# Kernel tuning notes

Hardware: AMD Instinct MI355X
Metric: run time of the kernel (lower is better)

## Reference

```python
import jax, jax.numpy as jnp
import numpy as np

B, N, D, H, MLP = 8, 1024, 1024, 16, 4096
DEPTH = D // H
EPS = 1e-6
INV_SQRT_DEPTH = 1.0 / np.sqrt(DEPTH).astype(np.float32)


def _linear_params(key, fan_in, fan_out):
    w = jax.random.normal(key, (fan_in, fan_out), dtype=jnp.float32) * 0.02
    b = jnp.zeros((fan_out,), dtype=jnp.float32)
    return w, b


def setup_inputs() -> dict:
    key = jax.random.key(0)
    ks = jax.random.split(key, 20)
    inp = {}
    inp['inputs'] = jax.random.normal(ks[0], (B, N, D), dtype=jnp.float32)
    inp['z'] = jax.random.normal(ks[1], (B, D), dtype=jnp.float32)
    # norm1 conditioning MLPs
    inp['n1_hw'], inp['n1_hb'] = _linear_params(ks[2], D, D)
    inp['n1_gw'], inp['n1_gb'] = _linear_params(ks[3], D, D)
    inp['n1_bw'], inp['n1_bb'] = _linear_params(ks[4], D, D)
    # attention
    inp['wq_w'], inp['wq_b'] = _linear_params(ks[5], D, D)
    inp['wk_w'], inp['wk_b'] = _linear_params(ks[6], D, D)
    inp['wv_w'], inp['wv_b'] = _linear_params(ks[7], D, D)
    inp['qa_w'], inp['qa_b'] = _linear_params(ks[8], D, H)
    inp['out_w'], inp['out_b'] = _linear_params(ks[9], D, D)
    # norm2 conditioning MLPs
    inp['n2_hw'], inp['n2_hb'] = _linear_params(ks[10], D, D)
    inp['n2_gw'], inp['n2_gb'] = _linear_params(ks[11], D, D)
    inp['n2_bw'], inp['n2_bb'] = _linear_params(ks[12], D, D)
    # MLP
    inp['mlp_w1'], inp['mlp_b1'] = _linear_params(ks[13], D, MLP)
    inp['mlp_w2'], inp['mlp_b2'] = _linear_params(ks[14], MLP, D)
    return inp


def _sm_norm(x, z, hw, hb, gw, gb, bw, bb):
    # LayerNorm over last dim, no affine
    mean = jnp.mean(x, axis=-1, keepdims=True)
    var = jnp.mean(jnp.square(x - mean), axis=-1, keepdims=True)
    xn = (x - mean) / jnp.sqrt(var + EPS)
    h = jax.nn.relu(z @ hw + hb)                 # [B, D]
    scale = (h @ gw + gb)[:, :, None]            # [B, D, 1]
    shift = (h @ bw + bb)[:, :, None]            # [B, D, 1]
    # broadcasts since N == D (as in the torch module)
    return xn * scale + shift


def _additive_attn(x, wq_w, wq_b, wk_w, wk_b, wv_w, wv_b, qa_w, qa_b, out_w, out_b):
    q = x @ wq_w + wq_b                          # [B, N, D]
    k = x @ wk_w + wk_b
    v = x @ wv_w + wv_b
    attn = jnp.transpose(q @ qa_w + qa_b, (0, 2, 1)) * INV_SQRT_DEPTH  # [B, H, N]
    attn = jax.nn.softmax(attn, axis=-1)
    qh = q.reshape(B, N, H, DEPTH).transpose(0, 2, 1, 3)  # [B, H, N, d]
    kh = k.reshape(B, N, H, DEPTH).transpose(0, 2, 1, 3)
    vh = v.reshape(B, N, H, DEPTH).transpose(0, 2, 1, 3)
    global_q = jnp.einsum('bhn,bhnd->bhd', attn, qh)[:, :, None, :]  # [B, H, 1, d]
    r = global_q * kh * vh                       # [B, H, N, d]
    r = r.transpose(0, 2, 1, 3).reshape(B, N, D)
    return r @ out_w + out_b, attn


def reference(inputs, z,
              n1_hw, n1_hb, n1_gw, n1_gb, n1_bw, n1_bb,
              wq_w, wq_b, wk_w, wk_b, wv_w, wv_b, qa_w, qa_b, out_w, out_b,
              n2_hw, n2_hb, n2_gw, n2_gb, n2_bw, n2_bb,
              mlp_w1, mlp_b1, mlp_w2, mlp_b2):
    x_norm1 = _sm_norm(inputs, z, n1_hw, n1_hb, n1_gw, n1_gb, n1_bw, n1_bb)
    attn_out, attn_maps = _additive_attn(x_norm1, wq_w, wq_b, wk_w, wk_b,
                                         wv_w, wv_b, qa_w, qa_b, out_w, out_b)
    attn_out = inputs + attn_out                 # dropout rate 0 -> identity
    x_norm2 = _sm_norm(attn_out, z, n2_hw, n2_hb, n2_gw, n2_gb, n2_bw, n2_bb)
    h = jax.nn.gelu(x_norm2 @ mlp_w1 + mlp_b1, approximate=False)
    mlp_out = h @ mlp_w2 + mlp_b2
    output = attn_out + mlp_out
    return output, attn_maps
```

## Files before the change

### kernel.cpp

```cpp
#include <hip/hip_runtime.h>
#include <math.h>


typedef __attribute__((ext_vector_type(8))) short short8;
typedef __attribute__((ext_vector_type(4))) float f32x4;

#define DEVI __device__ __forceinline__

DEVI unsigned short f2bf(float f) {
  union { float f; unsigned int u; } c; c.f = f;
  unsigned int r = c.u + 0x7fffu + ((c.u >> 16) & 1u);
  return (unsigned short)(r >> 16);
}
DEVI float bf2f(unsigned short u) {
  union { unsigned int u; float f; } c; c.u = ((unsigned int)u) << 16;
  return c.f;
}

DEVI void async16(const void* g, void* l) {
  __builtin_amdgcn_global_load_lds((const __attribute__((address_space(1))) void*)g,
                                   (__attribute__((address_space(3))) void*)l, 16, 0, 0);
}

__global__ void transpose_bf16_k(const float* __restrict__ in,
                                 unsigned short* __restrict__ out, int R, int C) {
  __shared__ float tile[32][33];
  const int c0 = blockIdx.x * 32, r0 = blockIdx.y * 32;
  const int tx = threadIdx.x, ty = threadIdx.y;
#pragma unroll
  for (int j = 0; j < 4; j++) {
    int r = r0 + ty + j * 8, c = c0 + tx;
    if (r < R && c < C) tile[ty + j * 8][tx] = in[(size_t)r * C + c];
  }
  __syncthreads();
#pragma unroll
  for (int j = 0; j < 4; j++) {
    int c = c0 + ty + j * 8, r = r0 + tx;
    if (c < C && r < R) out[(size_t)c * R + r] = f2bf(tile[tx][ty + j * 8]);
  }
}

__global__ void pad_bias_k(const float* __restrict__ qa_b, float* __restrict__ pad) {
  int t = threadIdx.x;
  pad[t] = (t < 16) ? qa_b[t] : 0.f;
}

__global__ void bias3_k(const float* __restrict__ b0, const float* __restrict__ b1,
                        const float* __restrict__ b2, float* __restrict__ out) {
  const int t = blockIdx.x * 256 + threadIdx.x;
  out[t] = (t < 1024) ? b0[t] : (t < 2048 ? b1[t - 1024] : b2[t - 2048]);
}

__global__ void zero_k(float4* __restrict__ p) {
  p[blockIdx.x * 256 + threadIdx.x] = float4{0.f, 0.f, 0.f, 0.f};
}

template <int NMAT>
__global__ __launch_bounds__(256) void skinny_k(const float* __restrict__ X,
                                                const float* __restrict__ W0,
                                                const float* __restrict__ W1,
                                                float* __restrict__ acc0,
                                                float* __restrict__ acc1) {
  const int tid = threadIdx.x;
  const int jt = blockIdx.x, kc = blockIdx.y;
  const int jl = tid & 63, kg = tid >> 6;
  const int jcol = jt * 64 + jl;
  __shared__ float xs[8][64];
  for (int i = tid; i < 512; i += 256) {
    const int b = i >> 6, kk = i & 63;
    xs[b][kk] = X[b * 1024 + kc * 64 + kk];
  }
  __syncthreads();
  float a0[8], a1[8];
#pragma unroll
  for (int b = 0; b < 8; b++) { a0[b] = 0.f; a1[b] = 0.f; }
#pragma unroll
  for (int kk = 0; kk < 16; kk++) {
    const int k = kg * 16 + kk;
    const float w0 = W0[(size_t)(kc * 64 + k) * 1024 + jcol];
#pragma unroll
    for (int b = 0; b < 8; b++) a0[b] += xs[b][k] * w0;
    if (NMAT == 2) {
      const float w1 = W1[(size_t)(kc * 64 + k) * 1024 + jcol];
#pragma unroll
      for (int b = 0; b < 8; b++) a1[b] += xs[b][k] * w1;
    }
  }
  __shared__ float red[256][9];
#pragma unroll
  for (int b = 0; b < 8; b++) red[tid][b] = a0[b];
  __syncthreads();
  if (tid < 64) {
#pragma unroll
    for (int b = 0; b < 8; b++) {
      const float s = red[tid][b] + red[tid + 64][b] + red[tid + 128][b] + red[tid + 192][b];
      atomicAdd(&acc0[b * 1024 + jcol], s);
    }
  }
  if (NMAT == 2) {
    __syncthreads();
#pragma unroll
    for (int b = 0; b < 8; b++) red[tid][b] = a1[b];
    __syncthreads();
    if (tid < 64) {
#pragma unroll
      for (int b = 0; b < 8; b++) {
        const float s = red[tid][b] + red[tid + 64][b] + red[tid + 128][b] + red[tid + 192][b];
        atomicAdd(&acc1[b * 1024 + jcol], s);
      }
    }
  }
}

__global__ void h_epi_k(const float* __restrict__ acc, const float* __restrict__ hb,
                        float* __restrict__ h) {
  const int i = blockIdx.x * 256 + threadIdx.x;
  h[i] = fmaxf(acc[i] + hb[i & 1023], 0.f);
}

__global__ __launch_bounds__(256) void ln_mod_k(const float* __restrict__ x,
                                                const float* __restrict__ s_acc,
                                                const float* __restrict__ t_acc,
                                                const float* __restrict__ gb,
                                                const float* __restrict__ bb,
                                                unsigned short* __restrict__ out) {
  const int lane = threadIdx.x & 63, wid = threadIdx.x >> 6;
  const size_t row = (size_t)blockIdx.x * 4 + wid;
  const int n = (int)(row & 1023);
  const float4* xr = (const float4*)(x + row * 1024);
  float4 v[4];
  float s = 0.f, ss = 0.f;
#pragma unroll
  for (int j = 0; j < 4; j++) {
    v[j] = xr[j * 64 + lane];
    s += v[j].x + v[j].y + v[j].z + v[j].w;
    ss += v[j].x * v[j].x + v[j].y * v[j].y + v[j].z * v[j].z + v[j].w * v[j].w;
  }
#pragma unroll
  for (int o = 32; o > 0; o >>= 1) { s += __shfl_xor(s, o); ss += __shfl_xor(ss, o); }
  const float mean = s * (1.f / 1024.f);
  const float var = ss * (1.f / 1024.f) - mean * mean;
  const float inv = rsqrtf(var + 1e-6f);
  const float scale = s_acc[row] + gb[n];
  const float shift = t_acc[row] + bb[n];
  const float sc = scale * inv;
  const float sh = shift - mean * sc;
#pragma unroll
  for (int j = 0; j < 4; j++) {
    ushort4 o4;
    o4.x = f2bf(v[j].x * sc + sh);
    o4.y = f2bf(v[j].y * sc + sh);
    o4.z = f2bf(v[j].z * sc + sh);
    o4.w = f2bf(v[j].w * sc + sh);
    *(ushort4*)(out + row * 1024 + (size_t)(j * 64 + lane) * 4) = o4;
  }
}

template <int EPI, int BM>
__global__ __launch_bounds__(512, 2) void gemm256(const unsigned short* __restrict__ A,
                                                  const unsigned short* __restrict__ BT,
                                                  const float* __restrict__ bias,
                                                  const float* __restrict__ resid,
                                                  void* __restrict__ Cout,
                                                  int M, int N, int K) {
  constexpr bool SWAP = (EPI == 0 || EPI == 1);
  constexpr int WROWS = BM / 2;
  constexpr int MF = WROWS / 16;
  constexpr int MPH = MF / 2;
  constexpr int ALOADS_H = (WROWS * 64) / (512 * 8);
  __shared__ unsigned short lds[2 * BM * 64 + 2 * 256 * 64];
  unsigned short* As0 = lds;
  unsigned short* Bs0 = lds + 2 * BM * 64;
  const int tid = threadIdx.x;
  const int lane = tid & 63, w = tid >> 6;
  const int wm = w >> 2, wn = w & 3;
  const int lr = lane & 15;
  const int g0 = lane >> 4;
  const size_t brow = (size_t)blockIdx.y * BM;
  const size_t bcol = (size_t)blockIdx.x * 256;
  const unsigned short* Ab = A + brow * (size_t)K;
  const unsigned short* Bb = BT + bcol * (size_t)K;
  const int NT = K >> 6;

  const f32x4 zero = {0.f, 0.f, 0.f, 0.f};
  f32x4 acc[MF][4];
#pragma unroll
  for (int m = 0; m < MF; m++)
#pragma unroll
    for (int n = 0; n < 4; n++) acc[m][n] = zero;

  auto stageA = [&](int t, int h) {
    const int d = t & 1, k0 = t << 6;
#pragma unroll
    for (int i = 0; i < ALOADS_H; i++) {
      const int c = i * 512 + tid;
      const int r = h * WROWS + (c >> 3), g = c & 7;
      const int gl = g ^ (r & 7);
      async16(Ab + (size_t)r * K + (k0 + gl * 8),
              &As0[(size_t)d * BM * 64 + (size_t)h * WROWS * 64 + c * 8]);
    }
  };
  auto stageB = [&](int t, int h) {
    const int d = t & 1, k0 = t << 6;
#pragma unroll
    for (int i = 0; i < 2; i++) {
      const int c = i * 512 + tid;
      const int r = h * 128 + (c >> 3), g = c & 7;
      const int gl = g ^ (r & 7);
      async16(Bb + (size_t)r * K + (k0 + gl * 8),
              &Bs0[(size_t)d * 256 * 64 + (size_t)h * 128 * 64 + c * 8]);
    }
  };

  stageA(0, 0); stageA(0, 1); stageB(0, 0); stageB(0, 1);

  for (int t = 0; t < NT; ++t) {
    const unsigned short* as = As0 + (size_t)(t & 1) * BM * 64;
    const unsigned short* bs = Bs0 + (size_t)(t & 1) * 256 * 64;
#pragma unroll
    for (int p = 0; p < 4; ++p) {
      if (t + 1 < NT) {
        if (p == 0) stageA(t + 1, 0);
        else if (p == 1) stageA(t + 1, 1);
        else if (p == 2) stageB(t + 1, 0);
        else stageB(t + 1, 1);
      }
      if (p == 0) {
        if (t + 1 < NT) {
          if constexpr (ALOADS_H == 2) asm volatile("s_waitcnt vmcnt(2)" ::: "memory");
          else asm volatile("s_waitcnt vmcnt(1)" ::: "memory");
        } else {
          asm volatile("s_waitcnt vmcnt(0)" ::: "memory");
        }
        __builtin_amdgcn_s_barrier();
      }
      const int mf0 = (p >> 1) * MPH;
      const int nf0 = (p & 1) * 2;
      short8 bfrag[2][2], afrag[2][MPH];
#pragma unroll
      for (int kki = 0; kki < 2; kki++) {
        const int gk = kki * 4 + g0;
#pragma unroll
        for (int nf = 0; nf < 2; nf++) {
          const int r = wn * 64 + (nf0 + nf) * 16 + lr;
          bfrag[kki][nf] = *(const short8*)&bs[r * 64 + ((gk ^ (r & 7)) << 3)];
        }
#pragma unroll
        for (int mf = 0; mf < MPH; mf++) {
          const int r = wm * WROWS + (mf0 + mf) * 16 + lr;
          afrag[kki][mf] = *(const short8*)&as[r * 64 + ((gk ^ (r & 7)) << 3)];
        }
      }
      __builtin_amdgcn_s_setprio(1);
#pragma unroll
      for (int kki = 0; kki < 2; kki++)
#pragma unroll
        for (int mf = 0; mf < MPH; mf++)
#pragma unroll
          for (int nf = 0; nf < 2; nf++) {
            if constexpr (SWAP)
              acc[mf0 + mf][nf0 + nf] = __builtin_amdgcn_mfma_f32_16x16x32_bf16(
                  bfrag[kki][nf], afrag[kki][mf], acc[mf0 + mf][nf0 + nf], 0, 0, 0);
            else
              acc[mf0 + mf][nf0 + nf] = __builtin_amdgcn_mfma_f32_16x16x32_bf16(
                  afrag[kki][mf], bfrag[kki][nf], acc[mf0 + mf][nf0 + nf], 0, 0, 0);
          }
      __builtin_amdgcn_s_setprio(0);
      __builtin_amdgcn_s_barrier();
    }
  }

  if constexpr (SWAP) {
    unsigned short* cst = lds;
    const int g4 = (lane >> 4) * 4;
#pragma unroll
    for (int nf = 0; nf < 4; nf++) {
#pragma unroll
      for (int mf = 0; mf < MF; mf++) {
        const int row = wm * WROWS + mf * 16 + lr;
        const int colb = wn * 64 + nf * 16 + g4;
        const float4 bv = *(const float4*)&bias[bcol + colb];
        float v[4];
#pragma unroll
        for (int j = 0; j < 4; j++) {
          v[j] = acc[mf][nf][j] + (&bv.x)[j];
          if (EPI == 1) v[j] = 0.5f * v[j] * (1.0f + erff(v[j] * 0.70710678118654752f));
        }
        ushort4 pck;
        pck.x = f2bf(v[0]); pck.y = f2bf(v[1]); pck.z = f2bf(v[2]); pck.w = f2bf(v[3]);
        const int byo = row * 512 + ((colb * 2) ^ ((row & 7) << 4));
        *(ushort4*)((char*)cst + byo) = pck;
      }
    }
    __syncthreads();
    unsigned short* outp;
    size_t ostride;
    if (EPI == 0) {
      outp = (unsigned short*)Cout + (size_t)(bcol >> 10) * ((size_t)M << 10) + (bcol & 1023);
      ostride = 1024;
    } else {
      outp = (unsigned short*)Cout + bcol;
      ostride = (size_t)N;
    }
#pragma unroll
    for (int it = 0; it < BM / 16; it++) {
      const int fl = it * 4096 + tid * 8;
      const int row = fl >> 8, colu = fl & 255;
      const int byo = row * 512 + ((colu * 2) ^ ((row & 7) << 4));
      const short8 val = *(const short8*)((char*)cst + byo);
      *(short8*)(outp + (size_t)(brow + row) * ostride + colu) = val;
    }
  } else {
    const int lc = lane & 15, lrow = (lane >> 4) * 4;
#pragma unroll
    for (int nf = 0; nf < 4; nf++) {
      const size_t col = bcol + wn * 64 + nf * 16 + lc;
      const float bv = bias[col];
#pragma unroll
      for (int mf = 0; mf < MF; mf++) {
#pragma unroll
        for (int j = 0; j < 4; j++) {
          const size_t row = brow + wm * WROWS + mf * 16 + lrow + j;
          const size_t idx = row * (size_t)N + col;
          ((float*)Cout)[idx] = acc[mf][nf][j] + bv + resid[idx];
        }
      }
    }
  }
}

template <int EPI>
__global__ __launch_bounds__(256) void gemm_bf16(const unsigned short* __restrict__ A,
                                                 const unsigned short* __restrict__ BT,
                                                 const float* __restrict__ bias,
                                                 const float* __restrict__ resid,
                                                 void* __restrict__ Cout,
                                                 int M, int N, int K) {
  __shared__ unsigned short As[128 * 64];
  __shared__ unsigned short Bs[128 * 64];
  const int tid = threadIdx.x;
  const int lane = tid & 63, wid = tid >> 6;
  const int wr = wid >> 1, wc = wid & 1;
  const size_t brow = (size_t)blockIdx.y * 128;
  const size_t bcol = (size_t)blockIdx.x * 128;
  const unsigned short* Ab = A + brow * (size_t)K;
  const unsigned short* Bb = BT + bcol * (size_t)K;

  const f32x4 zero = {0.f, 0.f, 0.f, 0.f};
  f32x4 acc[4][4];
#pragma unroll
  for (int m = 0; m < 4; m++)
#pragma unroll
    for (int n = 0; n < 4; n++) acc[m][n] = zero;

  for (int k0 = 0; k0 < K; k0 += 64) {
#pragma unroll
    for (int i = 0; i < 4; i++) {
      const int eo = (i * 256 + tid) * 8;
      const int r = eo >> 6, c = eo & 63;
      async16(Ab + (size_t)r * K + (k0 + c), &As[eo]);
      async16(Bb + (size_t)r * K + (k0 + c), &Bs[eo]);
    }
    __syncthreads();
    const int lr = lane & 15, lk = (lane >> 4) * 8;
#pragma unroll
    for (int kk = 0; kk < 64; kk += 32) {
      short8 af[4], bfv[4];
#pragma unroll
      for (int m = 0; m < 4; m++)
        af[m] = *(const short8*)&As[(wr * 64 + m * 16 + lr) * 64 + kk + lk];
#pragma unroll
      for (int n = 0; n < 4; n++)
        bfv[n] = *(const short8*)&Bs[(wc * 64 + n * 16 + lr) * 64 + kk + lk];
#pragma unroll
      for (int m = 0; m < 4; m++)
#pragma unroll
        for (int n = 0; n < 4; n++)
          acc[m][n] = __builtin_amdgcn_mfma_f32_16x16x32_bf16(af[m], bfv[n], acc[m][n], 0, 0, 0);
    }
    __syncthreads();
  }

  const int lc = lane & 15, lr4 = (lane >> 4) * 4;
#pragma unroll
  for (int n = 0; n < 4; n++) {
    const size_t col = bcol + wc * 64 + n * 16 + lc;
    const float bv = bias[col];
#pragma unroll
    for (int m = 0; m < 4; m++) {
#pragma unroll
      for (int j = 0; j < 4; j++) {
        const size_t row = brow + wr * 64 + m * 16 + lr4 + j;
        const size_t idx = row * (size_t)N + col;
        ((float*)Cout)[idx] = acc[m][n][j] + bv;
      }
    }
  }
}

__global__ __launch_bounds__(256) void softmax_k(const float* __restrict__ logits,
                                                 float* __restrict__ attn) {
  const int tid = threadIdx.x;
  const int bh = blockIdx.x;
  const int b = bh >> 4, h = bh & 15;
  __shared__ float redm[4];
  __shared__ float reds[4];
  float vals[4];
#pragma unroll
  for (int j = 0; j < 4; j++) {
    const int n = j * 256 + tid;
    vals[j] = logits[((size_t)b * 1024 + n) * 128 + h] * 0.125f;
  }
  float m = fmaxf(fmaxf(vals[0], vals[1]), fmaxf(vals[2], vals[3]));
#pragma unroll
  for (int o = 32; o > 0; o >>= 1) m = fmaxf(m, __shfl_xor(m, o));
  if ((tid & 63) == 0) redm[tid >> 6] = m;
  __syncthreads();
  m = fmaxf(fmaxf(redm[0], redm[1]), fmaxf(redm[2], redm[3]));
  float e[4];
  float s = 0.f;
#pragma unroll
  for (int j = 0; j < 4; j++) { e[j] = expf(vals[j] - m); s += e[j]; }
#pragma unroll
  for (int o = 32; o > 0; o >>= 1) s += __shfl_xor(s, o);
  if ((tid & 63) == 0) reds[tid >> 6] = s;
  __syncthreads();
  s = reds[0] + reds[1] + reds[2] + reds[3];
  const float invs = 1.f / s;
#pragma unroll
  for (int j = 0; j < 4; j++)
    attn[(size_t)bh * 1024 + j * 256 + tid] = e[j] * invs;
}

__global__ __launch_bounds__(256) void global_q_k(const float* __restrict__ attn,
                                                  const unsigned short* __restrict__ Q,
                                                  float* __restrict__ gq) {
  const int tid = threadIdx.x;
  const int bh = blockIdx.x;
  const int b = bh >> 4, h = bh & 15;
  const int d = tid & 63, g = tid >> 6;
  const float* arow = attn + (size_t)bh * 1024;
  const unsigned short* qcol = Q + (size_t)b * 1024 * 1024 + h * 64 + d;
  float acc = 0.f;
  for (int n = g * 256; n < g * 256 + 256; n++)
    acc += arow[n] * bf2f(qcol[(size_t)n * 1024]);
  __shared__ float red[256];
  red[tid] = acc;
  __syncthreads();
  if (g == 0) gq[(size_t)bh * 64 + d] = red[d] + red[64 + d] + red[128 + d] + red[192 + d];
}

__global__ __launch_bounds__(256) void r_k(const unsigned short* __restrict__ Kb,
                                           const unsigned short* __restrict__ Vb,
                                           const float* __restrict__ gq,
                                           unsigned short* __restrict__ R) {
  const size_t i = ((size_t)blockIdx.x * 256 + threadIdx.x) * 8;
  const int col = (int)(i & 1023);
  const size_t b = i >> 20;
  const int h = col >> 6, dd = col & 63;
  const float* g = gq + ((b << 4) + h) * 64 + dd;
  short8 kv = *(const short8*)(Kb + i);
  short8 vv = *(const short8*)(Vb + i);
  short8 r;
#pragma unroll
  for (int j = 0; j < 8; j++) {
    float f = g[j] * bf2f((unsigned short)kv[j]) * bf2f((unsigned short)vv[j]);
    r[j] = (short)f2bf(f);
  }
  *(short8*)(R + i) = r;
}

extern "C" void kernel_launch(void* const* d_in, const int* in_sizes, int n_in,
                              void* d_out, int out_size, void* d_ws, size_t ws_size,
                              hipStream_t stream) {
  (void)in_sizes; (void)n_in; (void)out_size; (void)ws_size;
  const float* inputs = (const float*)d_in[0];
  const float* z      = (const float*)d_in[1];
  const float* n1_hw = (const float*)d_in[2];  const float* n1_hb = (const float*)d_in[3];
  const float* n1_gw = (const float*)d_in[4];  const float* n1_gb = (const float*)d_in[5];
  const float* n1_bw = (const float*)d_in[6];  const float* n1_bb = (const float*)d_in[7];
  const float* wq_w  = (const float*)d_in[8];  const float* wq_b  = (const float*)d_in[9];
  const float* wk_w  = (const float*)d_in[10]; const float* wk_b  = (const float*)d_in[11];
  const float* wv_w  = (const float*)d_in[12]; const float* wv_b  = (const float*)d_in[13];
  const float* qa_w  = (const float*)d_in[14]; const float* qa_b  = (const float*)d_in[15];
  const float* out_w = (const float*)d_in[16]; const float* out_b = (const float*)d_in[17];
  const float* n2_hw = (const float*)d_in[18]; const float* n2_hb = (const float*)d_in[19];
  const float* n2_gw = (const float*)d_in[20]; const float* n2_gb = (const float*)d_in[21];
  const float* n2_bw = (const float*)d_in[22]; const float* n2_bb = (const float*)d_in[23];
  const float* mlp_w1 = (const float*)d_in[24]; const float* mlp_b1 = (const float*)d_in[25];
  const float* mlp_w2 = (const float*)d_in[26]; const float* mlp_b2 = (const float*)d_in[27];

  const int M = 8192, D = 1024, MLPD = 4096;

  char* ws = (char*)d_ws;
  size_t o = 0;
  auto alloc = [&](size_t bytes) -> char* {
    char* p = ws + o;
    o += (bytes + 255) & ~(size_t)255;
    return p;
  };
  unsigned short* wqkvT = (unsigned short*)alloc((size_t)3 * D * D * 2);
  unsigned short* woT = (unsigned short*)alloc((size_t)D * D * 2);
  unsigned short* w1T = (unsigned short*)alloc((size_t)MLPD * D * 2);
  unsigned short* w2T = (unsigned short*)alloc((size_t)D * MLPD * 2);
  unsigned short* qaT = (unsigned short*)alloc((size_t)128 * D * 2);
  unsigned short* xn  = (unsigned short*)alloc((size_t)M * D * 2);
  char* big = alloc((size_t)M * MLPD * 2);
  unsigned short* Qb = (unsigned short*)big;
  unsigned short* Kb = (unsigned short*)(big + (size_t)M * D * 2);
  unsigned short* Vb = (unsigned short*)(big + (size_t)M * D * 4);
  float* logits      = (float*)(big + (size_t)M * D * 6);
  unsigned short* hbuf = (unsigned short*)big;
  float* cacc  = (float*)alloc(6 * 8192 * 4);
  float* accH1 = cacc;
  float* accS1 = cacc + 1 * 8192;
  float* accT1 = cacc + 2 * 8192;
  float* accH2 = cacc + 3 * 8192;
  float* accS2 = cacc + 4 * 8192;
  float* accT2 = cacc + 5 * 8192;
  float* h1     = (float*)alloc(8 * 1024 * 4);
  float* h2     = (float*)alloc(8 * 1024 * 4);
  float* gq     = (float*)alloc(8 * 16 * 64 * 4);
  float* qa_b_pad = (float*)alloc(128 * 4);
  float* qkvb    = (float*)alloc(3072 * 4);

  float* out0 = (float*)d_out;
  float* attn = (float*)d_out + (size_t)M * D;

  const dim3 tb(32, 8);
  hipLaunchKernelGGL(transpose_bf16_k, dim3(32, 32), tb, 0, stream, wq_w, wqkvT, D, D);
  hipLaunchKernelGGL(transpose_bf16_k, dim3(32, 32), tb, 0, stream, wk_w, wqkvT + (size_t)D * D, D, D);
  hipLaunchKernelGGL(transpose_bf16_k, dim3(32, 32), tb, 0, stream, wv_w, wqkvT + (size_t)2 * D * D, D, D);
  hipLaunchKernelGGL(transpose_bf16_k, dim3(32, 32), tb, 0, stream, out_w, woT, D, D);
  hipLaunchKernelGGL(transpose_bf16_k, dim3(128, 32), tb, 0, stream, mlp_w1, w1T, D, MLPD);
  hipLaunchKernelGGL(transpose_bf16_k, dim3(32, 128), tb, 0, stream, mlp_w2, w2T, MLPD, D);
  hipLaunchKernelGGL(transpose_bf16_k, dim3(1, 32), tb, 0, stream, qa_w, qaT, D, 16);
  hipLaunchKernelGGL(pad_bias_k, dim3(1), dim3(128), 0, stream, qa_b, qa_b_pad);
  hipLaunchKernelGGL(bias3_k, dim3(12), dim3(256), 0, stream, wq_b, wk_b, wv_b, qkvb);

  hipLaunchKernelGGL(zero_k, dim3(48), dim3(256), 0, stream, (float4*)cacc);
  hipLaunchKernelGGL(skinny_k<1>, dim3(16, 16), dim3(256), 0, stream, z, n1_hw, (const float*)nullptr, accH1, (float*)nullptr);
  hipLaunchKernelGGL(h_epi_k, dim3(32), dim3(256), 0, stream, accH1, n1_hb, h1);
  hipLaunchKernelGGL(skinny_k<2>, dim3(16, 16), dim3(256), 0, stream, h1, n1_gw, n1_bw, accS1, accT1);
  hipLaunchKernelGGL(skinny_k<1>, dim3(16, 16), dim3(256), 0, stream, z, n2_hw, (const float*)nullptr, accH2, (float*)nullptr);
  hipLaunchKernelGGL(h_epi_k, dim3(32), dim3(256), 0, stream, accH2, n2_hb, h2);
  hipLaunchKernelGGL(skinny_k<2>, dim3(16, 16), dim3(256), 0, stream, h2, n2_gw, n2_bw, accS2, accT2);

  hipLaunchKernelGGL(ln_mod_k, dim3(M / 4), dim3(256), 0, stream, inputs, accS1, accT1, n1_gb, n1_bb, xn);

  hipLaunchKernelGGL((gemm256<0, 256>), dim3(12, 32), dim3(512), 0, stream, xn, wqkvT, qkvb, (const float*)nullptr, (void*)Qb, M, 3072, D);

  hipLaunchKernelGGL(gemm_bf16<3>, dim3(1, 64), dim3(256), 0, stream, Qb, qaT, qa_b_pad, (const float*)nullptr, (void*)logits, M, 128, D);

  hipLaunchKernelGGL(softmax_k, dim3(128), dim3(256), 0, stream, logits, attn);

  hipLaunchKernelGGL(global_q_k, dim3(128), dim3(256), 0, stream, attn, Qb, gq);

  hipLaunchKernelGGL(r_k, dim3(M * D / 8 / 256), dim3(256), 0, stream, Kb, Vb, gq, Kb);

  hipLaunchKernelGGL((gemm256<2, 128>), dim3(4, 64), dim3(512), 0, stream, Kb, woT, out_b, inputs, (void*)out0, M, D, D);

  hipLaunchKernelGGL(ln_mod_k, dim3(M / 4), dim3(256), 0, stream, out0, accS2, accT2, n2_gb, n2_bb, xn);

  hipLaunchKernelGGL((gemm256<1, 256>), dim3(16, 32), dim3(512), 0, stream, xn, w1T, mlp_b1, (const float*)nullptr, (void*)hbuf, M, MLPD, D);

  hipLaunchKernelGGL((gemm256<2, 128>), dim3(4, 64), dim3(512), 0, stream, hbuf, w2T, mlp_b2, out0, (void*)out0, M, D, MLPD);
}
```

Measured before the change: 647.4 us.

## Triple-buffer GEMM pipeline with fixed 128-row tiles; split-K logits GEMM with atomics

```diff
diff --git a/kernel.cpp b/kernel.cpp
--- a/kernel.cpp
+++ b/kernel.cpp
@@ -156,7 +156,7 @@
   }
 }
 
-template <int EPI, int BM>
+template <int EPI>
 __global__ __launch_bounds__(512, 2) void gemm256(const unsigned short* __restrict__ A,
                                                   const unsigned short* __restrict__ BT,
                                                   const float* __restrict__ bias,
@@ -164,106 +164,84 @@
                                                   void* __restrict__ Cout,
                                                   int M, int N, int K) {
   constexpr bool SWAP = (EPI == 0 || EPI == 1);
-  constexpr int WROWS = BM / 2;
-  constexpr int MF = WROWS / 16;
-  constexpr int MPH = MF / 2;
-  constexpr int ALOADS_H = (WROWS * 64) / (512 * 8);
-  __shared__ unsigned short lds[2 * BM * 64 + 2 * 256 * 64];
-  unsigned short* As0 = lds;
-  unsigned short* Bs0 = lds + 2 * BM * 64;
+  constexpr int BUF = 128 * 64 + 256 * 64;
+  __shared__ unsigned short lds[3 * BUF];
   const int tid = threadIdx.x;
   const int lane = tid & 63, w = tid >> 6;
   const int wm = w >> 2, wn = w & 3;
   const int lr = lane & 15;
   const int g0 = lane >> 4;
-  const size_t brow = (size_t)blockIdx.y * BM;
+  const size_t brow = (size_t)blockIdx.y * 128;
   const size_t bcol = (size_t)blockIdx.x * 256;
   const unsigned short* Ab = A + brow * (size_t)K;
   const unsigned short* Bb = BT + bcol * (size_t)K;
   const int NT = K >> 6;
 
   const f32x4 zero = {0.f, 0.f, 0.f, 0.f};
-  f32x4 acc[MF][4];
-#pragma unroll
-  for (int m = 0; m < MF; m++)
+  f32x4 acc[4][4];
+#pragma unroll
+  for (int m = 0; m < 4; m++)
 #pragma unroll
     for (int n = 0; n < 4; n++) acc[m][n] = zero;
 
-  auto stageA = [&](int t, int h) {
-    const int d = t & 1, k0 = t << 6;
-#pragma unroll
-    for (int i = 0; i < ALOADS_H; i++) {
-      const int c = i * 512 + tid;
-      const int r = h * WROWS + (c >> 3), g = c & 7;
+  auto stageH = [&](int t, int h) {
+    const int bufo = (t % 3) * BUF;
+    const int k0 = t << 6;
+    {
+      const int c = tid;
+      const int r = h * 64 + (c >> 3), g = c & 7;
       const int gl = g ^ (r & 7);
-      async16(Ab + (size_t)r * K + (k0 + gl * 8),
-              &As0[(size_t)d * BM * 64 + (size_t)h * WROWS * 64 + c * 8]);
-    }
-  };
-  auto stageB = [&](int t, int h) {
-    const int d = t & 1, k0 = t << 6;
+      async16(Ab + (size_t)r * K + (k0 + gl * 8), &lds[bufo + h * 64 * 64 + c * 8]);
+    }
 #pragma unroll
     for (int i = 0; i < 2; i++) {
       const int c = i * 512 + tid;
       const int r = h * 128 + (c >> 3), g = c & 7;
       const int gl = g ^ (r & 7);
       async16(Bb + (size_t)r * K + (k0 + gl * 8),
-              &Bs0[(size_t)d * 256 * 64 + (size_t)h * 128 * 64 + c * 8]);
+              &lds[bufo + 128 * 64 + h * 128 * 64 + c * 8]);
     }
   };
 
-  stageA(0, 0); stageA(0, 1); stageB(0, 0); stageB(0, 1);
+  stageH(0, 0); stageH(0, 1); stageH(1, 0); stageH(1, 1);
 
   for (int t = 0; t < NT; ++t) {
-    const unsigned short* as = As0 + (size_t)(t & 1) * BM * 64;
-    const unsigned short* bs = Bs0 + (size_t)(t & 1) * 256 * 64;
-#pragma unroll
-    for (int p = 0; p < 4; ++p) {
-      if (t + 1 < NT) {
-        if (p == 0) stageA(t + 1, 0);
-        else if (p == 1) stageA(t + 1, 1);
-        else if (p == 2) stageB(t + 1, 0);
-        else stageB(t + 1, 1);
-      }
-      if (p == 0) {
-        if (t + 1 < NT) {
-          if constexpr (ALOADS_H == 2) asm volatile("s_waitcnt vmcnt(2)" ::: "memory");
-          else asm volatile("s_waitcnt vmcnt(1)" ::: "memory");
-        } else {
-          asm volatile("s_waitcnt vmcnt(0)" ::: "memory");
-        }
-        __builtin_amdgcn_s_barrier();
-      }
-      const int mf0 = (p >> 1) * MPH;
-      const int nf0 = (p & 1) * 2;
-      short8 bfrag[2][2], afrag[2][MPH];
+    const unsigned short* as = &lds[(t % 3) * BUF];
+    const unsigned short* bs = as + 128 * 64;
+    if (t + 1 < NT) asm volatile("s_waitcnt vmcnt(6)" ::: "memory");
+    else asm volatile("s_waitcnt vmcnt(0)" ::: "memory");
+    __builtin_amdgcn_s_barrier();
+#pragma unroll
+    for (int p = 0; p < 2; ++p) {
+      if (t + 2 < NT) stageH(t + 2, p);
+      short8 afrag[2][2], bfrag[2][4];
 #pragma unroll
       for (int kki = 0; kki < 2; kki++) {
         const int gk = kki * 4 + g0;
 #pragma unroll
-        for (int nf = 0; nf < 2; nf++) {
-          const int r = wn * 64 + (nf0 + nf) * 16 + lr;
+        for (int m2 = 0; m2 < 2; m2++) {
+          const int r = wm * 64 + (p * 2 + m2) * 16 + lr;
+          afrag[kki][m2] = *(const short8*)&as[r * 64 + ((gk ^ (r & 7)) << 3)];
+        }
+#pragma unroll
+        for (int nf = 0; nf < 4; nf++) {
+          const int r = wn * 64 + nf * 16 + lr;
           bfrag[kki][nf] = *(const short8*)&bs[r * 64 + ((gk ^ (r & 7)) << 3)];
-        }
-#pragma unroll
-        for (int mf = 0; mf < MPH; mf++) {
-          const int r = wm * WROWS + (mf0 + mf) * 16 + lr;
-          afrag[kki][mf] = *(const short8*)&as[r * 64 + ((gk ^ (r & 7)) << 3)];
         }
       }
       __builtin_amdgcn_s_setprio(1);
 #pragma unroll
       for (int kki = 0; kki < 2; kki++)
 #pragma unroll
-        for (int mf = 0; mf < MPH; mf++)
-#pragma unroll
-          for (int nf = 0; nf < 2; nf++) {
+        for (int m2 = 0; m2 < 2; m2++)
+#pragma unroll
+          for (int nf = 0; nf < 4; nf++) {
             if constexpr (SWAP)
-              acc[mf0 + mf][nf0 + nf] = __builtin_amdgcn_mfma_f32_16x16x32_bf16(
-                  bfrag[kki][nf], afrag[kki][mf], acc[mf0 + mf][nf0 + nf], 0, 0, 0);
+              acc[p * 2 + m2][nf] = __builtin_amdgcn_mfma_f32_16x16x32_bf16(
+                  bfrag[kki][nf], afrag[kki][m2], acc[p * 2 + m2][nf], 0, 0, 0);
             else
-              acc[mf0 + mf][nf0 + nf] = __builtin_amdgcn_mfma_f32_16x16x32_bf16(
-                  afrag[kki][mf], bfrag[kki][nf], acc[mf0 + mf][nf0 + nf], 0, 0, 0);
+              acc[p * 2 + m2][nf] = __builtin_amdgcn_mfma_f32_16x16x32_bf16(
+                  afrag[kki][m2], bfrag[kki][nf], acc[p * 2 + m2][nf], 0, 0, 0);
           }
       __builtin_amdgcn_s_setprio(0);
       __builtin_amdgcn_s_barrier();
@@ -276,8 +254,8 @@
 #pragma unroll
     for (int nf = 0; nf < 4; nf++) {
 #pragma unroll
-      for (int mf = 0; mf < MF; mf++) {
-        const int row = wm * WROWS + mf * 16 + lr;
+      for (int mf = 0; mf < 4; mf++) {
+        const int row = wm * 64 + mf * 16 + lr;
         const int colb = wn * 64 + nf * 16 + g4;
         const float4 bv = *(const float4*)&bias[bcol + colb];
         float v[4];
@@ -303,7 +281,7 @@
       ostride = (size_t)N;
     }
 #pragma unroll
-    for (int it = 0; it < BM / 16; it++) {
+    for (int it = 0; it < 8; it++) {
       const int fl = it * 4096 + tid * 8;
       const int row = fl >> 8, colu = fl & 255;
       const int byo = row * 512 + ((colu * 2) ^ ((row & 7) << 4));
@@ -317,10 +295,10 @@
       const size_t col = bcol + wn * 64 + nf * 16 + lc;
       const float bv = bias[col];
 #pragma unroll
-      for (int mf = 0; mf < MF; mf++) {
+      for (int mf = 0; mf < 4; mf++) {
 #pragma unroll
         for (int j = 0; j < 4; j++) {
-          const size_t row = brow + wm * WROWS + mf * 16 + lrow + j;
+          const size_t row = brow + wm * 64 + mf * 16 + lrow + j;
           const size_t idx = row * (size_t)N + col;
           ((float*)Cout)[idx] = acc[mf][nf][j] + bv + resid[idx];
         }
@@ -329,22 +307,21 @@
   }
 }
 
-template <int EPI>
-__global__ __launch_bounds__(256) void gemm_bf16(const unsigned short* __restrict__ A,
-                                                 const unsigned short* __restrict__ BT,
-                                                 const float* __restrict__ bias,
-                                                 const float* __restrict__ resid,
-                                                 void* __restrict__ Cout,
-                                                 int M, int N, int K) {
+__global__ __launch_bounds__(256) void gemm_logits(const unsigned short* __restrict__ A,
+                                                   const unsigned short* __restrict__ BT,
+                                                   const float* __restrict__ bias,
+                                                   float* __restrict__ out,
+                                                   int M, int K) {
   __shared__ unsigned short As[128 * 64];
   __shared__ unsigned short Bs[128 * 64];
   const int tid = threadIdx.x;
   const int lane = tid & 63, wid = tid >> 6;
   const int wr = wid >> 1, wc = wid & 1;
+  const int kc = blockIdx.x;
+  const int KCH = K / gridDim.x;
   const size_t brow = (size_t)blockIdx.y * 128;
-  const size_t bcol = (size_t)blockIdx.x * 128;
   const unsigned short* Ab = A + brow * (size_t)K;
-  const unsigned short* Bb = BT + bcol * (size_t)K;
+  const unsigned short* Bb = BT;
 
   const f32x4 zero = {0.f, 0.f, 0.f, 0.f};
   f32x4 acc[4][4];
@@ -353,7 +330,7 @@
 #pragma unroll
     for (int n = 0; n < 4; n++) acc[m][n] = zero;
 
-  for (int k0 = 0; k0 < K; k0 += 64) {
+  for (int k0 = kc * KCH; k0 < (kc + 1) * KCH; k0 += 64) {
 #pragma unroll
     for (int i = 0; i < 4; i++) {
       const int eo = (i * 256 + tid) * 8;
@@ -384,15 +361,14 @@
   const int lc = lane & 15, lr4 = (lane >> 4) * 4;
 #pragma unroll
   for (int n = 0; n < 4; n++) {
-    const size_t col = bcol + wc * 64 + n * 16 + lc;
-    const float bv = bias[col];
+    const int col = wc * 64 + n * 16 + lc;
+    const float bv = (kc == 0) ? bias[col] : 0.f;
 #pragma unroll
     for (int m = 0; m < 4; m++) {
 #pragma unroll
       for (int j = 0; j < 4; j++) {
         const size_t row = brow + wr * 64 + m * 16 + lr4 + j;
-        const size_t idx = row * (size_t)N + col;
-        ((float*)Cout)[idx] = acc[m][n][j] + bv;
+        atomicAdd(&out[row * 128 + col], acc[m][n][j] + bv);
       }
     }
   }
@@ -539,6 +515,8 @@
   hipLaunchKernelGGL(bias3_k, dim3(12), dim3(256), 0, stream, wq_b, wk_b, wv_b, qkvb);
 
   hipLaunchKernelGGL(zero_k, dim3(48), dim3(256), 0, stream, (float4*)cacc);
+  hipLaunchKernelGGL(zero_k, dim3(1024), dim3(256), 0, stream, (float4*)logits);
+
   hipLaunchKernelGGL(skinny_k<1>, dim3(16, 16), dim3(256), 0, stream, z, n1_hw, (const float*)nullptr, accH1, (float*)nullptr);
   hipLaunchKernelGGL(h_epi_k, dim3(32), dim3(256), 0, stream, accH1, n1_hb, h1);
   hipLaunchKernelGGL(skinny_k<2>, dim3(16, 16), dim3(256), 0, stream, h1, n1_gw, n1_bw, accS1, accT1);
@@ -548,9 +526,9 @@
 
   hipLaunchKernelGGL(ln_mod_k, dim3(M / 4), dim3(256), 0, stream, inputs, accS1, accT1, n1_gb, n1_bb, xn);
 
-  hipLaunchKernelGGL((gemm256<0, 256>), dim3(12, 32), dim3(512), 0, stream, xn, wqkvT, qkvb, (const float*)nullptr, (void*)Qb, M, 3072, D);
-
-  hipLaunchKernelGGL(gemm_bf16<3>, dim3(1, 64), dim3(256), 0, stream, Qb, qaT, qa_b_pad, (const float*)nullptr, (void*)logits, M, 128, D);
+  hipLaunchKernelGGL(gemm256<0>, dim3(12, 64), dim3(512), 0, stream, xn, wqkvT, qkvb, (const float*)nullptr, (void*)Qb, M, 3072, D);
+
+  hipLaunchKernelGGL(gemm_logits, dim3(4, 64), dim3(256), 0, stream, Qb, qaT, qa_b_pad, logits, M, D);
 
   hipLaunchKernelGGL(softmax_k, dim3(128), dim3(256), 0, stream, logits, attn);
 
@@ -558,11 +536,11 @@
 
   hipLaunchKernelGGL(r_k, dim3(M * D / 8 / 256), dim3(256), 0, stream, Kb, Vb, gq, Kb);
 
-  hipLaunchKernelGGL((gemm256<2, 128>), dim3(4, 64), dim3(512), 0, stream, Kb, woT, out_b, inputs, (void*)out0, M, D, D);
+  hipLaunchKernelGGL(gemm256<2>, dim3(4, 64), dim3(512), 0, stream, Kb, woT, out_b, inputs, (void*)out0, M, D, D);
 
   hipLaunchKernelGGL(ln_mod_k, dim3(M / 4), dim3(256), 0, stream, out0, accS2, accT2, n2_gb, n2_bb, xn);
 
-  hipLaunchKernelGGL((gemm256<1, 256>), dim3(16, 32), dim3(512), 0, stream, xn, w1T, mlp_b1, (const float*)nullptr, (void*)hbuf, M, MLPD, D);
-
-  hipLaunchKernelGGL((gemm256<2, 128>), dim3(4, 64), dim3(512), 0, stream, hbuf, w2T, mlp_b2, out0, (void*)out0, M, D, MLPD);
-}
+  hipLaunchKernelGGL(gemm256<1>, dim3(16, 64), dim3(512), 0, stream, xn, w1T, mlp_b1, (const float*)nullptr, (void*)hbuf, M, MLPD, D);
+
+  hipLaunchKernelGGL(gemm256<2>, dim3(4, 64), dim3(512), 0, stream, hbuf, w2T, mlp_b2, out0, (void*)out0, M, D, MLPD);
+}
```

After: 635.9 us. Within noise of the previous version (-1.8%).
